# Kernel tuning notes

Measured on AMD Instinct MI355X. Metric: run time of the kernel, lower is better.

Reference implementation:

```python
import jax, jax.numpy as jnp
import numpy as np

B, N, C_IN, C_H, C_OUT, R, X_DIM = 32, 256, 64, 128, 128, 5, 1024
NEG = -9e15

def _leaky(x, s=0.2):
    return jnp.where(x >= 0, x, s * x)

def gat_layer(atoms, mask, W, b, a):
    # atoms: (B,n,c_in), mask: (B,n,n,R) bool, W: (c_in, R*c), b: (R*c,), a: (R, 2c)
    bs, n, _ = atoms.shape
    c = a.shape[1] // 2
    h = (atoms @ W + b).reshape(bs, n, R, c)            # (B,n,R,c)
    src = jnp.einsum('bnrc,rc->bnr', h, a[:, :c])       # a . h_i part
    dst = jnp.einsum('bnrc,rc->bnr', h, a[:, c:])       # a . h_j part
    logits = _leaky(src[:, :, None, :] + dst[:, None, :, :])  # (B,i,j,R)
    masked = jnp.where(mask, logits, NEG)
    probs = jax.nn.softmax(masked.reshape(bs, n, n * R), axis=2).reshape(bs, n, n, R)
    return jnp.einsum('bijr,bjrc->bic', probs, h)       # (B,n,c)

def setup_inputs() -> dict:
    key = jax.random.key(0)
    ks = jax.random.split(key, 16)
    def p(k, shape, fan):
        return jax.random.normal(k, shape, jnp.float32) * (1.414 / np.sqrt(fan))
    inp = {
        'x': jax.random.normal(ks[0], (B, X_DIM), jnp.float32),
        'y_atoms': jax.random.normal(ks[1], (B, N, C_IN), jnp.float32),
        'y_bonds': jax.random.randint(ks[2], (B, N, N, R), 0, 2, jnp.int32),
        'W1': p(ks[3], (C_IN, R * C_H), C_IN), 'b1': jnp.zeros((R * C_H,), jnp.float32),
        'a1': p(ks[4], (R, 2 * C_H), 2 * C_H),
        'W2': p(ks[5], (C_H, R * C_H), C_H), 'b2': jnp.zeros((R * C_H,), jnp.float32),
        'a2': p(ks[6], (R, 2 * C_H), 2 * C_H),
        'W3': p(ks[7], (C_H, R * C_OUT), C_H), 'b3': jnp.zeros((R * C_OUT,), jnp.float32),
        'a3': p(ks[8], (R, 2 * C_OUT), 2 * C_OUT),
        'We1': p(ks[9], (2 * C_OUT + X_DIM, 256), 2 * C_OUT + X_DIM), 'be1': jnp.zeros((256,), jnp.float32),
        'We2': p(ks[10], (256, 32), 256), 'be2': jnp.zeros((32,), jnp.float32),
        'We3': p(ks[11], (32, 1), 32), 'be3': jnp.zeros((1,), jnp.float32),
    }
    return inp

def reference(x, y_atoms, y_bonds, W1, b1, a1, W2, b2, a2, W3, b3, a3,
              We1, be1, We2, be2, We3, be3):
    mask = (y_bonds == 1)
    h = gat_layer(y_atoms, mask, W1, b1, a1)
    h = _leaky(h)                                   # dropout is identity at eval
    h = gat_layer(h, mask, W2, b2, a2)
    h = _leaky(h)
    h = gat_layer(h, mask, W3, b3, a3)
    y_feats = jnp.concatenate([jnp.mean(h, axis=1), jnp.max(h, axis=1)], axis=1)
    z = jnp.concatenate([x, y_feats], axis=1)
    z = _leaky(z @ We1 + be1)
    z = _leaky(z @ We2 + be2)
    return z @ We3 + be3
```

## Files before the change

kernel.cpp:

```cpp
#include <hip/hip_runtime.h>
#include <cstddef>

#define BB 32
#define NN 256
#define RR 5

typedef __attribute__((ext_vector_type(8))) short bf16x8;
typedef __attribute__((ext_vector_type(4))) float f32x4;

__device__ __forceinline__ float lrelu(float x) { return x >= 0.f ? x : 0.2f * x; }
__device__ __forceinline__ unsigned short f2bf(float x) {
    unsigned u = __float_as_uint(x);
    u += 0x7FFFu + ((u >> 16) & 1u);
    return (unsigned short)(u >> 16);
}

__global__ __launch_bounds__(256) void k_prep(const float* __restrict__ W1,
                                              const float* __restrict__ W2,
                                              const float* __restrict__ W3,
                                              const float* __restrict__ We1,
                                              const int* __restrict__ bonds,
                                              unsigned short* __restrict__ WT1,
                                              unsigned short* __restrict__ WT2,
                                              unsigned short* __restrict__ WT3,
                                              float* __restrict__ We1T,
                                              unsigned char* __restrict__ maskp) {
    __shared__ float Ls[40][256];
    int blk = blockIdx.x;
    int t = threadIdx.x;
    if (blk < 30) {
        int layer = blk / 10, nt = blk % 10;
        const float* W;
        unsigned short* WT;
        int K;
        if (layer == 0)      { W = W1; WT = WT1; K = 64; }
        else if (layer == 1) { W = W2; WT = WT2; K = 128; }
        else                 { W = W3; WT = WT3; K = 128; }
        int n = nt * 64 + (t & 63);
        for (int kg = (int)(t >> 6); kg < K / 8; kg += 4) {
            bf16x8 v;
#pragma unroll
            for (int e = 0; e < 8; ++e) v[e] = (short)f2bf(W[(size_t)(kg * 8 + e) * 640 + n]);
            *(bf16x8*)&WT[(size_t)n * K + kg * 8] = v;
        }
    } else if (blk < 62) {
        int bt = blk - 30;
        for (int kk = 0; kk < 40; ++kk)
            Ls[kk][t] = We1[(size_t)(bt * 40 + kk) * 256 + t];
        __syncthreads();
#pragma unroll
        for (int q = 0; q < 10; ++q) {
            float4 v;
            v.x = Ls[q * 4 + 0][t]; v.y = Ls[q * 4 + 1][t];
            v.z = Ls[q * 4 + 2][t]; v.w = Ls[q * 4 + 3][t];
            *(float4*)&We1T[(size_t)t * 1280 + bt * 40 + q * 4] = v;
        }
    } else {
        int idx = (blk - 62) * 256 + t;
        const int* p = bonds + (size_t)idx * 5;
        unsigned m = 0;
#pragma unroll
        for (int r = 0; r < 5; ++r) m |= (p[r] == 1) ? (1u << r) : 0u;
        maskp[idx] = (unsigned char)m;
    }
}

template <int K, int MODE>
__global__ __launch_bounds__(256) void k_gemm_h(const float* __restrict__ Af32,
                                                const float* __restrict__ aggP,
                                                const float* __restrict__ Zpart,
                                                const unsigned short* __restrict__ WTg,
                                                const float* __restrict__ bias,
                                                const float* __restrict__ avec,
                                                float* __restrict__ srcp,
                                                float* __restrict__ dstp,
                                                unsigned short* __restrict__ hTf) {
    const int t = threadIdx.x;
    const int n0 = blockIdx.x * 64, m0 = blockIdx.y * 64;
    const int w = t >> 6, lane = t & 63;
    const int colg = lane & 15, rquad = lane >> 4;
    const int m = m0 + w * 16 + colg;
    const int koff = rquad * 8;

    float zi = 0.f;
    if (MODE == 1) zi = 1.f / (Zpart[m] + Zpart[8192 + m]);

    f32x4 acc[4] = {};
#pragma unroll
    for (int kk = 0; kk < K; kk += 32) {
        bf16x8 af;
        size_t off = (size_t)m * K + kk + koff;
        if (MODE == 1) {
            float4 a0 = *(const float4*)&aggP[off];
            float4 a1 = *(const float4*)&aggP[off + 4];
            float4 b0 = *(const float4*)&aggP[off + 1048576];
            float4 b1 = *(const float4*)&aggP[off + 1048576 + 4];
            af[0] = (short)f2bf(lrelu((a0.x + b0.x) * zi));
            af[1] = (short)f2bf(lrelu((a0.y + b0.y) * zi));
            af[2] = (short)f2bf(lrelu((a0.z + b0.z) * zi));
            af[3] = (short)f2bf(lrelu((a0.w + b0.w) * zi));
            af[4] = (short)f2bf(lrelu((a1.x + b1.x) * zi));
            af[5] = (short)f2bf(lrelu((a1.y + b1.y) * zi));
            af[6] = (short)f2bf(lrelu((a1.z + b1.z) * zi));
            af[7] = (short)f2bf(lrelu((a1.w + b1.w) * zi));
        } else {
            float4 q0 = *(const float4*)&Af32[off];
            float4 q1 = *(const float4*)&Af32[off + 4];
            af[0] = (short)f2bf(q0.x); af[1] = (short)f2bf(q0.y);
            af[2] = (short)f2bf(q0.z); af[3] = (short)f2bf(q0.w);
            af[4] = (short)f2bf(q1.x); af[5] = (short)f2bf(q1.y);
            af[6] = (short)f2bf(q1.z); af[7] = (short)f2bf(q1.w);
        }
#pragma unroll
        for (int ct = 0; ct < 4; ++ct) {
            bf16x8 bfv = *(const bf16x8*)&WTg[(size_t)(n0 + ct * 16 + colg) * K + kk + koff];
            acc[ct] = __builtin_amdgcn_mfma_f32_16x16x32_bf16(af, bfv, acc[ct], 0, 0, 0);
        }
    }

    const int r = n0 >> 7, chalf = n0 & 127;
    const int b = m0 >> 8, jb = m0 & 255;
    float val[4][4];
    float ssum[4] = {0.f, 0.f, 0.f, 0.f}, dsum[4] = {0.f, 0.f, 0.f, 0.f};
#pragma unroll
    for (int ct = 0; ct < 4; ++ct) {
        int cg = chalf + ct * 16 + colg;
        float bv = bias[n0 + ct * 16 + colg];
        float asr = avec[r * 256 + cg];
        float ads = avec[r * 256 + 128 + cg];
#pragma unroll
        for (int reg = 0; reg < 4; ++reg) {
            float v = acc[ct][reg] + bv;
            val[ct][reg] = v;
            ssum[reg] += v * asr;
            dsum[reg] += v * ads;
        }
    }
#pragma unroll
    for (int mk = 1; mk < 16; mk <<= 1)
#pragma unroll
        for (int reg = 0; reg < 4; ++reg) {
            ssum[reg] += __shfl_xor(ssum[reg], mk);
            dsum[reg] += __shfl_xor(dsum[reg], mk);
        }
    if (colg == 0) {
        int half = (n0 >> 6) & 1;
#pragma unroll
        for (int reg = 0; reg < 4; ++reg) {
            int row = m0 + w * 16 + rquad * 4 + reg;
            srcp[half * 40960 + row * 5 + r] = ssum[reg];
            dstp[half * 40960 + row * 5 + r] = dsum[reg];
        }
    }
    {
        const int joct = (jb >> 3) + w * 2 + (rquad >> 1);
        const size_t tile = (size_t)((b * 5 + r) * 32 + joct) * 1024;
        const int sub = (rquad & 1) * 4;
#pragma unroll
        for (int ct = 0; ct < 4; ++ct) {
            int c = chalf + ct * 16 + colg;
            uint2 pk;
            pk.x = (unsigned)f2bf(val[ct][0]) | ((unsigned)f2bf(val[ct][1]) << 16);
            pk.y = (unsigned)f2bf(val[ct][2]) | ((unsigned)f2bf(val[ct][3]) << 16);
            *(uint2*)&hTf[tile + (size_t)c * 8 + sub] = pk;
        }
    }
}

__global__ __launch_bounds__(512) void k_agg(const unsigned short* __restrict__ hTf,
                                             const float* __restrict__ srcp,
                                             const float* __restrict__ dstp,
                                             const unsigned char* __restrict__ maskp,
                                             float* __restrict__ aggP,
                                             float* __restrict__ Zpart) {
    __shared__ unsigned short Ps[20480];
    __shared__ float Ss[160], Ds2l[640], Zrow[32];
    const int t = threadIdx.x;
    const int js = blockIdx.x, itile = blockIdx.y, b = blockIdx.z;
    const int ib = b * 256 + itile * 32;

    if (t < 160) Ss[t] = srcp[(size_t)ib * 5 + t] + srcp[40960 + (size_t)ib * 5 + t];
    if (t >= 160 && t < 192) Zrow[t - 160] = 0.f;
    for (int idx = t; idx < 640; idx += 512) {
        int jl = idx & 127, rr = idx >> 7;
        size_t o = (size_t)(b * 256 + js * 128 + jl) * 5 + rr;
        Ds2l[rr * 128 + jl] = dstp[o] + dstp[40960 + o];
    }
    __syncthreads();

#pragma unroll
    for (int it = 0; it < 5; ++it) {
        int p = it * 512 + t;
        int lane8 = p & 63, chunkrow = p >> 6;
        int colg8 = lane8 & 15, kq = lane8 >> 4;
        int ih = (chunkrow >= 20) ? 1 : 0;
        int s = chunkrow - ih * 20;
        int i = ih * 16 + colg8;
        int rr = s >> 2;
        int j0l = (s & 3) * 32 + kq * 8;
        uint2 mk8 = *(const uint2*)&maskp[((size_t)(ib + i) << 8) + js * 128 + j0l];
        float sv = Ss[i * 5 + rr];
        float esum = 0.f;
        bf16x8 pv;
#pragma unroll
        for (int e = 0; e < 8; ++e) {
            unsigned mb = ((e < 4 ? (mk8.x >> (8 * e)) : (mk8.y >> (8 * (e - 4)))) >> rr) & 1u;
            float v = lrelu(sv + Ds2l[rr * 128 + j0l + e]);
            float ev = mb ? __expf(v) : 0.f;
            unsigned short q = f2bf(ev);
            pv[e] = (short)q;
            esum += __uint_as_float((unsigned)q << 16);
        }
        *(bf16x8*)&Ps[p * 8] = pv;
        atomicAdd(&Zrow[i], esum);
    }
    __syncthreads();
    if (t < 32) Zpart[(size_t)js * 8192 + ib + t] = Zrow[t];

    const int w = t >> 6, lane = t & 63;
    const int ih = w & 1, ch = w >> 1;
    const int colg = lane & 15, rquad = lane >> 4;
    f32x4 acc[2] = {};
    const size_t bbase = (size_t)(b * 5) * 32 * 1024;
#pragma unroll
    for (int s = 0; s < 20; ++s) {
        bf16x8 af = *(const bf16x8*)&Ps[((ih * 20 + s) * 64 + lane) * 8];
        const int rr = s >> 2;
        const int joct = js * 16 + (s & 3) * 4 + rquad;
        const size_t tbase = bbase + (size_t)(rr * 32 + joct) * 1024;
#pragma unroll
        for (int ct = 0; ct < 2; ++ct) {
            int c = ch * 32 + ct * 16 + colg;
            bf16x8 bfv = *(const bf16x8*)&hTf[tbase + (size_t)c * 8];
            acc[ct] = __builtin_amdgcn_mfma_f32_16x16x32_bf16(af, bfv, acc[ct], 0, 0, 0);
        }
    }
    float* op = aggP + (size_t)js * 1048576;
    const int irow = ib + ih * 16 + rquad * 4;
#pragma unroll
    for (int ct = 0; ct < 2; ++ct) {
        int c = ch * 32 + ct * 16 + colg;
#pragma unroll
        for (int reg = 0; reg < 4; ++reg)
            op[(size_t)(irow + reg) * 128 + c] = acc[ct][reg];
    }
}

__global__ __launch_bounds__(256) void k_pool(const float* __restrict__ aggP,
                                              const float* __restrict__ Zpart,
                                              float* __restrict__ poolS,
                                              float* __restrict__ poolM) {
    int nc = blockIdx.x, b = blockIdx.y;
    int t = threadIdx.x;
    int c = t & 127, sub = t >> 7;
    __shared__ float Zl[32];
    __shared__ float Sh[2][128], Mh[2][128];
    if (t < 32) {
        int rowg = b * 256 + nc * 32 + t;
        Zl[t] = 1.f / (Zpart[rowg] + Zpart[8192 + rowg]);
    }
    __syncthreads();
    float sm = 0.f, mx = -3.4e38f;
#pragma unroll
    for (int nn = 0; nn < 16; ++nn) {
        int nl = sub * 16 + nn;
        size_t o = (size_t)(b * 256 + nc * 32 + nl) * 128 + c;
        float v = (aggP[o] + aggP[o + 1048576]) * Zl[nl];
        sm += v; mx = fmaxf(mx, v);
    }
    Sh[sub][c] = sm; Mh[sub][c] = mx;
    __syncthreads();
    if (t < 128) {
        poolS[(b * 8 + nc) * 128 + t] = Sh[0][t] + Sh[1][t];
        poolM[(b * 8 + nc) * 128 + t] = fmaxf(Mh[0][t], Mh[1][t]);
    }
}

__global__ __launch_bounds__(256) void k_mlp1(const float* __restrict__ x,
                                              const float* __restrict__ poolS,
                                              const float* __restrict__ poolM,
                                              const float* __restrict__ We1T,
                                              const float* __restrict__ be1,
                                              float* __restrict__ z1g) {
    int og = blockIdx.x, b = blockIdx.y;
    int t = threadIdx.x;
    __shared__ float zs[1280];
    for (int i = t; i < 1024; i += 256) zs[i] = x[b * 1024 + i];
    if (t < 128) {
        float s = 0.f;
#pragma unroll
        for (int nc = 0; nc < 8; ++nc) s += poolS[(b * 8 + nc) * 128 + t];
        zs[1024 + t] = s * (1.f / 256.f);
    } else {
        int f = t - 128;
        float mx = -3.4e38f;
#pragma unroll
        for (int nc = 0; nc < 8; ++nc) mx = fmaxf(mx, poolM[(b * 8 + nc) * 128 + f]);
        zs[1152 + f] = mx;
    }
    __syncthreads();
    int w = t >> 6, lane = t & 63;
#pragma unroll
    for (int oo = 0; oo < 4; ++oo) {
        int o = og * 16 + w * 4 + oo;
        float s = 0.f;
#pragma unroll
        for (int i = 0; i < 20; ++i) {
            int k = i * 64 + lane;
            s += zs[k] * We1T[(size_t)o * 1280 + k];
        }
#pragma unroll
        for (int off = 32; off > 0; off >>= 1) s += __shfl_down(s, off);
        if (lane == 0) z1g[b * 256 + o] = lrelu(s + be1[o]);
    }
}

__global__ __launch_bounds__(256) void k_mlp23(const float* __restrict__ z1g,
                                               const float* __restrict__ We2,
                                               const float* __restrict__ be2,
                                               const float* __restrict__ We3,
                                               const float* __restrict__ be3,
                                               float* __restrict__ out) {
    int b = blockIdx.x, t = threadIdx.x;
    __shared__ float zs[256], z2s[32];
    zs[t] = z1g[b * 256 + t];
    __syncthreads();
    if (t < 32) {
        float s2 = be2[t];
        for (int k = 0; k < 256; ++k) s2 += zs[k] * We2[k * 32 + t];
        z2s[t] = lrelu(s2);
    }
    __syncthreads();
    if (t == 0) {
        float s3 = be3[0];
#pragma unroll
        for (int k = 0; k < 32; ++k) s3 += z2s[k] * We3[k];
        out[b] = s3;
    }
}

constexpr size_t O_MASK  = 0;
constexpr size_t O_SRCP  = 2097152;
constexpr size_t O_DSTP  = O_SRCP + 2ull * 40960 * 4;
constexpr size_t O_AGG   = O_DSTP + 2ull * 40960 * 4;
constexpr size_t O_ZP    = O_AGG + 2ull * 1048576 * 4;
constexpr size_t O_HT    = O_ZP + 2ull * 8192 * 4;
constexpr size_t O_WT1   = O_HT + 5242880ull * 2;
constexpr size_t O_WT2   = O_WT1 + 640ull * 64 * 2;
constexpr size_t O_WT3   = O_WT2 + 640ull * 128 * 2;
constexpr size_t O_WE1T  = O_WT3 + 640ull * 128 * 2;
constexpr size_t O_POOLS = O_WE1T + 256ull * 1280 * 4;
constexpr size_t O_POOLM = O_POOLS + 32ull * 8 * 128 * 4;
constexpr size_t O_Z1    = O_POOLM + 32ull * 8 * 128 * 4;

extern "C" void kernel_launch(void* const* d_in, const int* in_sizes, int n_in,
                              void* d_out, int out_size, void* d_ws, size_t ws_size,
                              hipStream_t stream) {
    const float* x       = (const float*)d_in[0];
    const float* y_atoms = (const float*)d_in[1];
    const int*   y_bonds = (const int*)d_in[2];
    const float* W1 = (const float*)d_in[3];
    const float* b1 = (const float*)d_in[4];
    const float* a1 = (const float*)d_in[5];
    const float* W2 = (const float*)d_in[6];
    const float* b2 = (const float*)d_in[7];
    const float* a2 = (const float*)d_in[8];
    const float* W3 = (const float*)d_in[9];
    const float* b3 = (const float*)d_in[10];
    const float* a3 = (const float*)d_in[11];
    const float* We1 = (const float*)d_in[12];
    const float* be1 = (const float*)d_in[13];
    const float* We2 = (const float*)d_in[14];
    const float* be2 = (const float*)d_in[15];
    const float* We3 = (const float*)d_in[16];
    const float* be3 = (const float*)d_in[17];
    float* out = (float*)d_out;

    char* ws = (char*)d_ws;
    unsigned char* maskp = (unsigned char*)(ws + O_MASK);
    float* srcp = (float*)(ws + O_SRCP);
    float* dstp = (float*)(ws + O_DSTP);
    float* aggP = (float*)(ws + O_AGG);
    float* Zpart = (float*)(ws + O_ZP);
    unsigned short* hTf = (unsigned short*)(ws + O_HT);
    unsigned short* WT1 = (unsigned short*)(ws + O_WT1);
    unsigned short* WT2 = (unsigned short*)(ws + O_WT2);
    unsigned short* WT3 = (unsigned short*)(ws + O_WT3);
    float* We1T  = (float*)(ws + O_WE1T);
    float* poolS = (float*)(ws + O_POOLS);
    float* poolM = (float*)(ws + O_POOLM);
    float* z1g   = (float*)(ws + O_Z1);

    dim3 blk(256);

    k_prep<<<8254, blk, 0, stream>>>(W1, W2, W3, We1, y_bonds, WT1, WT2, WT3, We1T, maskp);

    k_gemm_h<64, 0><<<dim3(10, 128), blk, 0, stream>>>(
        y_atoms, nullptr, nullptr, WT1, b1, a1, srcp, dstp, hTf);
    k_agg<<<dim3(2, 8, 32), dim3(512), 0, stream>>>(hTf, srcp, dstp, maskp, aggP, Zpart);

    k_gemm_h<128, 1><<<dim3(10, 128), blk, 0, stream>>>(
        nullptr, aggP, Zpart, WT2, b2, a2, srcp, dstp, hTf);
    k_agg<<<dim3(2, 8, 32), dim3(512), 0, stream>>>(hTf, srcp, dstp, maskp, aggP, Zpart);

    k_gemm_h<128, 1><<<dim3(10, 128), blk, 0, stream>>>(
        nullptr, aggP, Zpart, WT3, b3, a3, srcp, dstp, hTf);
    k_agg<<<dim3(2, 8, 32), dim3(512), 0, stream>>>(hTf, srcp, dstp, maskp, aggP, Zpart);

    k_pool<<<dim3(8, 32), blk, 0, stream>>>(aggP, Zpart, poolS, poolM);
    k_mlp1<<<dim3(16, 32), blk, 0, stream>>>(x, poolS, poolM, We1T, be1, z1g);
    k_mlp23<<<32, blk, 0, stream>>>(z1g, We2, be2, We3, be3, out);
}
```

Baseline: 233.5 us.

## Fuse all GAT stages into one cooperative persistent kernel with grid syncs

Replaces the chain of eleven separate kernel launches (prep, three gemm/agg pairs, pool, two MLP kernels) with a single cooperative persistent kernel. Stages are separated by grid.sync() and work is distributed over virtual blocks in grid-stride loops. The mask packing is also vectorized to write 8 bytes per thread. This removes per-launch overhead and inter-kernel gaps. In exchange it adds grid-wide barrier cost and caps the grid at occupancy-limited size, which can cut parallelism in the gemm and agg phases.

```diff
diff --git a/kernel.cpp b/kernel.cpp
--- a/kernel.cpp
+++ b/kernel.cpp
@@ -1,9 +1,8 @@
 #include <hip/hip_runtime.h>
+#include <hip/hip_cooperative_groups.h>
 #include <cstddef>
 
-#define BB 32
-#define NN 256
-#define RR 5
+namespace cg = cooperative_groups;
 
 typedef __attribute__((ext_vector_type(8))) short bf16x8;
 typedef __attribute__((ext_vector_type(4))) float f32x4;
@@ -15,327 +14,370 @@
     return (unsigned short)(u >> 16);
 }
 
-__global__ __launch_bounds__(256) void k_prep(const float* __restrict__ W1,
-                                              const float* __restrict__ W2,
-                                              const float* __restrict__ W3,
-                                              const float* __restrict__ We1,
-                                              const int* __restrict__ bonds,
-                                              unsigned short* __restrict__ WT1,
-                                              unsigned short* __restrict__ WT2,
-                                              unsigned short* __restrict__ WT3,
-                                              float* __restrict__ We1T,
-                                              unsigned char* __restrict__ maskp) {
-    __shared__ float Ls[40][256];
-    int blk = blockIdx.x;
-    int t = threadIdx.x;
-    if (blk < 30) {
-        int layer = blk / 10, nt = blk % 10;
-        const float* W;
-        unsigned short* WT;
-        int K;
-        if (layer == 0)      { W = W1; WT = WT1; K = 64; }
-        else if (layer == 1) { W = W2; WT = WT2; K = 128; }
-        else                 { W = W3; WT = WT3; K = 128; }
-        int n = nt * 64 + (t & 63);
-        for (int kg = (int)(t >> 6); kg < K / 8; kg += 4) {
-            bf16x8 v;
-#pragma unroll
-            for (int e = 0; e < 8; ++e) v[e] = (short)f2bf(W[(size_t)(kg * 8 + e) * 640 + n]);
-            *(bf16x8*)&WT[(size_t)n * K + kg * 8] = v;
-        }
-    } else if (blk < 62) {
-        int bt = blk - 30;
-        for (int kk = 0; kk < 40; ++kk)
-            Ls[kk][t] = We1[(size_t)(bt * 40 + kk) * 256 + t];
-        __syncthreads();
-#pragma unroll
-        for (int q = 0; q < 10; ++q) {
-            float4 v;
-            v.x = Ls[q * 4 + 0][t]; v.y = Ls[q * 4 + 1][t];
-            v.z = Ls[q * 4 + 2][t]; v.w = Ls[q * 4 + 3][t];
-            *(float4*)&We1T[(size_t)t * 1280 + bt * 40 + q * 4] = v;
-        }
-    } else {
-        int idx = (blk - 62) * 256 + t;
-        const int* p = bonds + (size_t)idx * 5;
-        unsigned m = 0;
-#pragma unroll
-        for (int r = 0; r < 5; ++r) m |= (p[r] == 1) ? (1u << r) : 0u;
-        maskp[idx] = (unsigned char)m;
+template <int K, int MODE>
+__device__ __forceinline__ void gemm_phase(
+    int blk, int nvb, int t,
+    const float* __restrict__ Af32, const float* __restrict__ aggP,
+    const float* __restrict__ Zpart, const unsigned short* __restrict__ WTg,
+    const float* __restrict__ bias, const float* __restrict__ avec,
+    float* __restrict__ srcp, float* __restrict__ dstp,
+    unsigned short* __restrict__ hTf)
+{
+    const int su = t >> 8, tl = t & 255;
+    const int w = tl >> 6, lane = tl & 63;
+    const int colg = lane & 15, rquad = lane >> 4;
+    const int koff = rquad * 8;
+    for (int U = blk * 2 + su; U < 1280; U += nvb * 2) {
+        const int n0 = (U >> 7) * 64, m0 = (U & 127) * 64;
+        const int m = m0 + w * 16 + colg;
+        float zi = 0.f;
+        if (MODE == 1) zi = 1.f / (Zpart[m] + Zpart[8192 + m]);
+        f32x4 acc[4] = {};
+#pragma unroll
+        for (int kk = 0; kk < K; kk += 32) {
+            bf16x8 af;
+            size_t off = (size_t)m * K + kk + koff;
+            if (MODE == 1) {
+                float4 a0 = *(const float4*)&aggP[off];
+                float4 a1 = *(const float4*)&aggP[off + 4];
+                float4 b0 = *(const float4*)&aggP[off + 1048576];
+                float4 b1 = *(const float4*)&aggP[off + 1048576 + 4];
+                af[0] = (short)f2bf(lrelu((a0.x + b0.x) * zi));
+                af[1] = (short)f2bf(lrelu((a0.y + b0.y) * zi));
+                af[2] = (short)f2bf(lrelu((a0.z + b0.z) * zi));
+                af[3] = (short)f2bf(lrelu((a0.w + b0.w) * zi));
+                af[4] = (short)f2bf(lrelu((a1.x + b1.x) * zi));
+                af[5] = (short)f2bf(lrelu((a1.y + b1.y) * zi));
+                af[6] = (short)f2bf(lrelu((a1.z + b1.z) * zi));
+                af[7] = (short)f2bf(lrelu((a1.w + b1.w) * zi));
+            } else {
+                float4 q0 = *(const float4*)&Af32[off];
+                float4 q1 = *(const float4*)&Af32[off + 4];
+                af[0] = (short)f2bf(q0.x); af[1] = (short)f2bf(q0.y);
+                af[2] = (short)f2bf(q0.z); af[3] = (short)f2bf(q0.w);
+                af[4] = (short)f2bf(q1.x); af[5] = (short)f2bf(q1.y);
+                af[6] = (short)f2bf(q1.z); af[7] = (short)f2bf(q1.w);
+            }
+#pragma unroll
+            for (int ct = 0; ct < 4; ++ct) {
+                bf16x8 bfv = *(const bf16x8*)&WTg[(size_t)(n0 + ct * 16 + colg) * K + kk + koff];
+                acc[ct] = __builtin_amdgcn_mfma_f32_16x16x32_bf16(af, bfv, acc[ct], 0, 0, 0);
+            }
+        }
+        const int r = n0 >> 7, chalf = n0 & 127;
+        const int b = m0 >> 8, jb = m0 & 255;
+        float val[4][4];
+        float ssum[4] = {0.f, 0.f, 0.f, 0.f}, dsum[4] = {0.f, 0.f, 0.f, 0.f};
+#pragma unroll
+        for (int ct = 0; ct < 4; ++ct) {
+            int cg2 = chalf + ct * 16 + colg;
+            float bv = bias[n0 + ct * 16 + colg];
+            float asr = avec[r * 256 + cg2];
+            float ads = avec[r * 256 + 128 + cg2];
+#pragma unroll
+            for (int reg = 0; reg < 4; ++reg) {
+                float v = acc[ct][reg] + bv;
+                val[ct][reg] = v;
+                ssum[reg] += v * asr;
+                dsum[reg] += v * ads;
+            }
+        }
+#pragma unroll
+        for (int mk = 1; mk < 16; mk <<= 1)
+#pragma unroll
+            for (int reg = 0; reg < 4; ++reg) {
+                ssum[reg] += __shfl_xor(ssum[reg], mk);
+                dsum[reg] += __shfl_xor(dsum[reg], mk);
+            }
+        if (colg == 0) {
+            int half = (n0 >> 6) & 1;
+#pragma unroll
+            for (int reg = 0; reg < 4; ++reg) {
+                int row = m0 + w * 16 + rquad * 4 + reg;
+                srcp[half * 40960 + row * 5 + r] = ssum[reg];
+                dstp[half * 40960 + row * 5 + r] = dsum[reg];
+            }
+        }
+        {
+            const int joct = (jb >> 3) + w * 2 + (rquad >> 1);
+            const size_t tile = (size_t)((b * 5 + r) * 32 + joct) * 1024;
+            const int sub = (rquad & 1) * 4;
+#pragma unroll
+            for (int ct = 0; ct < 4; ++ct) {
+                int c = chalf + ct * 16 + colg;
+                uint2 pk;
+                pk.x = (unsigned)f2bf(val[ct][0]) | ((unsigned)f2bf(val[ct][1]) << 16);
+                pk.y = (unsigned)f2bf(val[ct][2]) | ((unsigned)f2bf(val[ct][3]) << 16);
+                *(uint2*)&hTf[tile + (size_t)c * 8 + sub] = pk;
+            }
+        }
     }
 }
 
-template <int K, int MODE>
-__global__ __launch_bounds__(256) void k_gemm_h(const float* __restrict__ Af32,
-                                                const float* __restrict__ aggP,
-                                                const float* __restrict__ Zpart,
-                                                const unsigned short* __restrict__ WTg,
-                                                const float* __restrict__ bias,
-                                                const float* __restrict__ avec,
-                                                float* __restrict__ srcp,
-                                                float* __restrict__ dstp,
-                                                unsigned short* __restrict__ hTf) {
-    const int t = threadIdx.x;
-    const int n0 = blockIdx.x * 64, m0 = blockIdx.y * 64;
-    const int w = t >> 6, lane = t & 63;
-    const int colg = lane & 15, rquad = lane >> 4;
-    const int m = m0 + w * 16 + colg;
-    const int koff = rquad * 8;
-
-    float zi = 0.f;
-    if (MODE == 1) zi = 1.f / (Zpart[m] + Zpart[8192 + m]);
-
-    f32x4 acc[4] = {};
-#pragma unroll
-    for (int kk = 0; kk < K; kk += 32) {
-        bf16x8 af;
-        size_t off = (size_t)m * K + kk + koff;
-        if (MODE == 1) {
-            float4 a0 = *(const float4*)&aggP[off];
-            float4 a1 = *(const float4*)&aggP[off + 4];
-            float4 b0 = *(const float4*)&aggP[off + 1048576];
-            float4 b1 = *(const float4*)&aggP[off + 1048576 + 4];
-            af[0] = (short)f2bf(lrelu((a0.x + b0.x) * zi));
-            af[1] = (short)f2bf(lrelu((a0.y + b0.y) * zi));
-            af[2] = (short)f2bf(lrelu((a0.z + b0.z) * zi));
-            af[3] = (short)f2bf(lrelu((a0.w + b0.w) * zi));
-            af[4] = (short)f2bf(lrelu((a1.x + b1.x) * zi));
-            af[5] = (short)f2bf(lrelu((a1.y + b1.y) * zi));
-            af[6] = (short)f2bf(lrelu((a1.z + b1.z) * zi));
-            af[7] = (short)f2bf(lrelu((a1.w + b1.w) * zi));
-        } else {
-            float4 q0 = *(const float4*)&Af32[off];
-            float4 q1 = *(const float4*)&Af32[off + 4];
-            af[0] = (short)f2bf(q0.x); af[1] = (short)f2bf(q0.y);
-            af[2] = (short)f2bf(q0.z); af[3] = (short)f2bf(q0.w);
-            af[4] = (short)f2bf(q1.x); af[5] = (short)f2bf(q1.y);
-            af[6] = (short)f2bf(q1.z); af[7] = (short)f2bf(q1.w);
-        }
-#pragma unroll
-        for (int ct = 0; ct < 4; ++ct) {
-            bf16x8 bfv = *(const bf16x8*)&WTg[(size_t)(n0 + ct * 16 + colg) * K + kk + koff];
-            acc[ct] = __builtin_amdgcn_mfma_f32_16x16x32_bf16(af, bfv, acc[ct], 0, 0, 0);
-        }
-    }
-
-    const int r = n0 >> 7, chalf = n0 & 127;
-    const int b = m0 >> 8, jb = m0 & 255;
-    float val[4][4];
-    float ssum[4] = {0.f, 0.f, 0.f, 0.f}, dsum[4] = {0.f, 0.f, 0.f, 0.f};
-#pragma unroll
-    for (int ct = 0; ct < 4; ++ct) {
-        int cg = chalf + ct * 16 + colg;
-        float bv = bias[n0 + ct * 16 + colg];
-        float asr = avec[r * 256 + cg];
-        float ads = avec[r * 256 + 128 + cg];
-#pragma unroll
-        for (int reg = 0; reg < 4; ++reg) {
-            float v = acc[ct][reg] + bv;
-            val[ct][reg] = v;
-            ssum[reg] += v * asr;
-            dsum[reg] += v * ads;
-        }
-    }
-#pragma unroll
-    for (int mk = 1; mk < 16; mk <<= 1)
-#pragma unroll
-        for (int reg = 0; reg < 4; ++reg) {
-            ssum[reg] += __shfl_xor(ssum[reg], mk);
-            dsum[reg] += __shfl_xor(dsum[reg], mk);
-        }
-    if (colg == 0) {
-        int half = (n0 >> 6) & 1;
-#pragma unroll
-        for (int reg = 0; reg < 4; ++reg) {
-            int row = m0 + w * 16 + rquad * 4 + reg;
-            srcp[half * 40960 + row * 5 + r] = ssum[reg];
-            dstp[half * 40960 + row * 5 + r] = dsum[reg];
-        }
-    }
-    {
-        const int joct = (jb >> 3) + w * 2 + (rquad >> 1);
-        const size_t tile = (size_t)((b * 5 + r) * 32 + joct) * 1024;
-        const int sub = (rquad & 1) * 4;
-#pragma unroll
-        for (int ct = 0; ct < 4; ++ct) {
-            int c = chalf + ct * 16 + colg;
-            uint2 pk;
-            pk.x = (unsigned)f2bf(val[ct][0]) | ((unsigned)f2bf(val[ct][1]) << 16);
-            pk.y = (unsigned)f2bf(val[ct][2]) | ((unsigned)f2bf(val[ct][3]) << 16);
-            *(uint2*)&hTf[tile + (size_t)c * 8 + sub] = pk;
-        }
-    }
-}
-
-__global__ __launch_bounds__(512) void k_agg(const unsigned short* __restrict__ hTf,
-                                             const float* __restrict__ srcp,
-                                             const float* __restrict__ dstp,
-                                             const unsigned char* __restrict__ maskp,
-                                             float* __restrict__ aggP,
-                                             float* __restrict__ Zpart) {
-    __shared__ unsigned short Ps[20480];
-    __shared__ float Ss[160], Ds2l[640], Zrow[32];
-    const int t = threadIdx.x;
-    const int js = blockIdx.x, itile = blockIdx.y, b = blockIdx.z;
-    const int ib = b * 256 + itile * 32;
-
-    if (t < 160) Ss[t] = srcp[(size_t)ib * 5 + t] + srcp[40960 + (size_t)ib * 5 + t];
-    if (t >= 160 && t < 192) Zrow[t - 160] = 0.f;
-    for (int idx = t; idx < 640; idx += 512) {
-        int jl = idx & 127, rr = idx >> 7;
-        size_t o = (size_t)(b * 256 + js * 128 + jl) * 5 + rr;
-        Ds2l[rr * 128 + jl] = dstp[o] + dstp[40960 + o];
-    }
-    __syncthreads();
-
-#pragma unroll
-    for (int it = 0; it < 5; ++it) {
-        int p = it * 512 + t;
-        int lane8 = p & 63, chunkrow = p >> 6;
-        int colg8 = lane8 & 15, kq = lane8 >> 4;
-        int ih = (chunkrow >= 20) ? 1 : 0;
-        int s = chunkrow - ih * 20;
-        int i = ih * 16 + colg8;
-        int rr = s >> 2;
-        int j0l = (s & 3) * 32 + kq * 8;
-        uint2 mk8 = *(const uint2*)&maskp[((size_t)(ib + i) << 8) + js * 128 + j0l];
-        float sv = Ss[i * 5 + rr];
-        float esum = 0.f;
-        bf16x8 pv;
-#pragma unroll
-        for (int e = 0; e < 8; ++e) {
-            unsigned mb = ((e < 4 ? (mk8.x >> (8 * e)) : (mk8.y >> (8 * (e - 4)))) >> rr) & 1u;
-            float v = lrelu(sv + Ds2l[rr * 128 + j0l + e]);
-            float ev = mb ? __expf(v) : 0.f;
-            unsigned short q = f2bf(ev);
-            pv[e] = (short)q;
-            esum += __uint_as_float((unsigned)q << 16);
-        }
-        *(bf16x8*)&Ps[p * 8] = pv;
-        atomicAdd(&Zrow[i], esum);
-    }
-    __syncthreads();
-    if (t < 32) Zpart[(size_t)js * 8192 + ib + t] = Zrow[t];
-
-    const int w = t >> 6, lane = t & 63;
-    const int ih = w & 1, ch = w >> 1;
-    const int colg = lane & 15, rquad = lane >> 4;
-    f32x4 acc[2] = {};
-    const size_t bbase = (size_t)(b * 5) * 32 * 1024;
-#pragma unroll
-    for (int s = 0; s < 20; ++s) {
-        bf16x8 af = *(const bf16x8*)&Ps[((ih * 20 + s) * 64 + lane) * 8];
-        const int rr = s >> 2;
-        const int joct = js * 16 + (s & 3) * 4 + rquad;
-        const size_t tbase = bbase + (size_t)(rr * 32 + joct) * 1024;
+__device__ __forceinline__ void agg_phase(
+    int blk, int nvb, int t, char* smem,
+    const unsigned short* __restrict__ hTf,
+    const float* __restrict__ srcp, const float* __restrict__ dstp,
+    const unsigned char* __restrict__ maskp,
+    float* __restrict__ aggP, float* __restrict__ Zpart)
+{
+    unsigned short* Ps = (unsigned short*)smem;
+    float* Ss = (float*)(smem + 40960);
+    float* Ds2l = (float*)(smem + 41600);
+    float* Zrow = (float*)(smem + 44160);
+    for (int vb = blk; vb < 512; vb += nvb) {
+        const int js = vb & 1, itile = (vb >> 1) & 7, b = vb >> 4;
+        const int ib = b * 256 + itile * 32;
+        __syncthreads();
+        if (t < 160) Ss[t] = srcp[(size_t)ib * 5 + t] + srcp[40960 + (size_t)ib * 5 + t];
+        if (t >= 160 && t < 192) Zrow[t - 160] = 0.f;
+        for (int idx = t; idx < 640; idx += 512) {
+            int jl = idx & 127, rr = idx >> 7;
+            size_t o = (size_t)(b * 256 + js * 128 + jl) * 5 + rr;
+            Ds2l[rr * 128 + jl] = dstp[o] + dstp[40960 + o];
+        }
+        __syncthreads();
+#pragma unroll
+        for (int it = 0; it < 5; ++it) {
+            int p = it * 512 + t;
+            int lane8 = p & 63, chunkrow = p >> 6;
+            int colg8 = lane8 & 15, kq = lane8 >> 4;
+            int ih = (chunkrow >= 20) ? 1 : 0;
+            int s = chunkrow - ih * 20;
+            int i = ih * 16 + colg8;
+            int rr = s >> 2;
+            int j0l = (s & 3) * 32 + kq * 8;
+            uint2 mk8 = *(const uint2*)&maskp[((size_t)(ib + i) << 8) + js * 128 + j0l];
+            float sv = Ss[i * 5 + rr];
+            float esum = 0.f;
+            bf16x8 pv;
+#pragma unroll
+            for (int e = 0; e < 8; ++e) {
+                unsigned mb = ((e < 4 ? (mk8.x >> (8 * e)) : (mk8.y >> (8 * (e - 4)))) >> rr) & 1u;
+                float v = lrelu(sv + Ds2l[rr * 128 + j0l + e]);
+                float ev = mb ? __expf(v) : 0.f;
+                unsigned short q = f2bf(ev);
+                pv[e] = (short)q;
+                esum += __uint_as_float((unsigned)q << 16);
+            }
+            *(bf16x8*)&Ps[p * 8] = pv;
+            atomicAdd(&Zrow[i], esum);
+        }
+        __syncthreads();
+        if (t < 32) Zpart[(size_t)js * 8192 + ib + t] = Zrow[t];
+
+        const int w = t >> 6, lane = t & 63;
+        const int ih = w & 1, ch = w >> 1;
+        const int colg = lane & 15, rquad = lane >> 4;
+        f32x4 acc[2] = {};
+        const size_t bbase = (size_t)(b * 5) * 32 * 1024;
+#pragma unroll
+        for (int s = 0; s < 20; ++s) {
+            bf16x8 af = *(const bf16x8*)&Ps[((ih * 20 + s) * 64 + lane) * 8];
+            const int rr = s >> 2;
+            const int joct = js * 16 + (s & 3) * 4 + rquad;
+            const size_t tbase = bbase + (size_t)(rr * 32 + joct) * 1024;
+#pragma unroll
+            for (int ct = 0; ct < 2; ++ct) {
+                int c = ch * 32 + ct * 16 + colg;
+                bf16x8 bfv = *(const bf16x8*)&hTf[tbase + (size_t)c * 8];
+                acc[ct] = __builtin_amdgcn_mfma_f32_16x16x32_bf16(af, bfv, acc[ct], 0, 0, 0);
+            }
+        }
+        float* op = aggP + (size_t)js * 1048576;
+        const int irow = ib + ih * 16 + rquad * 4;
 #pragma unroll
         for (int ct = 0; ct < 2; ++ct) {
             int c = ch * 32 + ct * 16 + colg;
-            bf16x8 bfv = *(const bf16x8*)&hTf[tbase + (size_t)c * 8];
-            acc[ct] = __builtin_amdgcn_mfma_f32_16x16x32_bf16(af, bfv, acc[ct], 0, 0, 0);
-        }
-    }
-    float* op = aggP + (size_t)js * 1048576;
-    const int irow = ib + ih * 16 + rquad * 4;
-#pragma unroll
-    for (int ct = 0; ct < 2; ++ct) {
-        int c = ch * 32 + ct * 16 + colg;
-#pragma unroll
-        for (int reg = 0; reg < 4; ++reg)
-            op[(size_t)(irow + reg) * 128 + c] = acc[ct][reg];
+#pragma unroll
+            for (int reg = 0; reg < 4; ++reg)
+                op[(size_t)(irow + reg) * 128 + c] = acc[ct][reg];
+        }
     }
 }
 
-__global__ __launch_bounds__(256) void k_pool(const float* __restrict__ aggP,
-                                              const float* __restrict__ Zpart,
-                                              float* __restrict__ poolS,
-                                              float* __restrict__ poolM) {
-    int nc = blockIdx.x, b = blockIdx.y;
-    int t = threadIdx.x;
-    int c = t & 127, sub = t >> 7;
-    __shared__ float Zl[32];
-    __shared__ float Sh[2][128], Mh[2][128];
-    if (t < 32) {
-        int rowg = b * 256 + nc * 32 + t;
-        Zl[t] = 1.f / (Zpart[rowg] + Zpart[8192 + rowg]);
-    }
-    __syncthreads();
-    float sm = 0.f, mx = -3.4e38f;
-#pragma unroll
-    for (int nn = 0; nn < 16; ++nn) {
-        int nl = sub * 16 + nn;
-        size_t o = (size_t)(b * 256 + nc * 32 + nl) * 128 + c;
-        float v = (aggP[o] + aggP[o + 1048576]) * Zl[nl];
-        sm += v; mx = fmaxf(mx, v);
-    }
-    Sh[sub][c] = sm; Mh[sub][c] = mx;
-    __syncthreads();
-    if (t < 128) {
-        poolS[(b * 8 + nc) * 128 + t] = Sh[0][t] + Sh[1][t];
-        poolM[(b * 8 + nc) * 128 + t] = fmaxf(Mh[0][t], Mh[1][t]);
-    }
-}
-
-__global__ __launch_bounds__(256) void k_mlp1(const float* __restrict__ x,
-                                              const float* __restrict__ poolS,
-                                              const float* __restrict__ poolM,
-                                              const float* __restrict__ We1T,
-                                              const float* __restrict__ be1,
-                                              float* __restrict__ z1g) {
-    int og = blockIdx.x, b = blockIdx.y;
-    int t = threadIdx.x;
-    __shared__ float zs[1280];
-    for (int i = t; i < 1024; i += 256) zs[i] = x[b * 1024 + i];
-    if (t < 128) {
-        float s = 0.f;
-#pragma unroll
-        for (int nc = 0; nc < 8; ++nc) s += poolS[(b * 8 + nc) * 128 + t];
-        zs[1024 + t] = s * (1.f / 256.f);
-    } else {
-        int f = t - 128;
-        float mx = -3.4e38f;
-#pragma unroll
-        for (int nc = 0; nc < 8; ++nc) mx = fmaxf(mx, poolM[(b * 8 + nc) * 128 + f]);
-        zs[1152 + f] = mx;
-    }
-    __syncthreads();
-    int w = t >> 6, lane = t & 63;
-#pragma unroll
-    for (int oo = 0; oo < 4; ++oo) {
-        int o = og * 16 + w * 4 + oo;
-        float s = 0.f;
-#pragma unroll
-        for (int i = 0; i < 20; ++i) {
-            int k = i * 64 + lane;
-            s += zs[k] * We1T[(size_t)o * 1280 + k];
-        }
-#pragma unroll
-        for (int off = 32; off > 0; off >>= 1) s += __shfl_down(s, off);
-        if (lane == 0) z1g[b * 256 + o] = lrelu(s + be1[o]);
-    }
-}
-
-__global__ __launch_bounds__(256) void k_mlp23(const float* __restrict__ z1g,
-                                               const float* __restrict__ We2,
-                                               const float* __restrict__ be2,
-                                               const float* __restrict__ We3,
-                                               const float* __restrict__ be3,
-                                               float* __restrict__ out) {
-    int b = blockIdx.x, t = threadIdx.x;
-    __shared__ float zs[256], z2s[32];
-    zs[t] = z1g[b * 256 + t];
-    __syncthreads();
-    if (t < 32) {
-        float s2 = be2[t];
-        for (int k = 0; k < 256; ++k) s2 += zs[k] * We2[k * 32 + t];
-        z2s[t] = lrelu(s2);
-    }
-    __syncthreads();
-    if (t == 0) {
-        float s3 = be3[0];
-#pragma unroll
-        for (int k = 0; k < 32; ++k) s3 += z2s[k] * We3[k];
-        out[b] = s3;
+__global__ __launch_bounds__(512, 4) void k_mega(
+    const float* __restrict__ x, const float* __restrict__ y_atoms,
+    const int* __restrict__ bonds,
+    const float* __restrict__ W1, const float* __restrict__ b1, const float* __restrict__ a1,
+    const float* __restrict__ W2, const float* __restrict__ b2, const float* __restrict__ a2,
+    const float* __restrict__ W3, const float* __restrict__ b3, const float* __restrict__ a3,
+    const float* __restrict__ We1, const float* __restrict__ be1,
+    const float* __restrict__ We2, const float* __restrict__ be2,
+    const float* __restrict__ We3, const float* __restrict__ be3,
+    unsigned short* __restrict__ WT1, unsigned short* __restrict__ WT2,
+    unsigned short* __restrict__ WT3, float* __restrict__ We1T,
+    unsigned char* __restrict__ maskp,
+    float* __restrict__ srcp, float* __restrict__ dstp,
+    float* __restrict__ aggP, float* __restrict__ Zpart,
+    unsigned short* __restrict__ hTf,
+    float* __restrict__ poolS, float* __restrict__ poolM,
+    float* __restrict__ z1g, float* __restrict__ out)
+{
+    __shared__ __align__(16) char smem[44288];
+    cg::grid_group grid = cg::this_grid();
+    const int blk = blockIdx.x;
+    const int nvb = gridDim.x;
+    const int t = threadIdx.x;
+
+    for (int vb = blk; vb < 62; vb += nvb) {
+        if (vb < 30) {
+            if (t < 256) {
+                int layer = vb / 10, nt = vb % 10;
+                const float* W; unsigned short* WT; int K;
+                if (layer == 0)      { W = W1; WT = WT1; K = 64; }
+                else if (layer == 1) { W = W2; WT = WT2; K = 128; }
+                else                 { W = W3; WT = WT3; K = 128; }
+                int n = nt * 64 + (t & 63);
+                for (int kg = (t >> 6); kg < K / 8; kg += 4) {
+                    bf16x8 v;
+#pragma unroll
+                    for (int e = 0; e < 8; ++e) v[e] = (short)f2bf(W[(size_t)(kg * 8 + e) * 640 + n]);
+                    *(bf16x8*)&WT[(size_t)n * K + kg * 8] = v;
+                }
+            }
+        } else {
+            int bt = vb - 30;
+            float* Ls = (float*)smem;
+            __syncthreads();
+            if (t < 256) {
+                for (int kk = 0; kk < 40; ++kk)
+                    Ls[kk * 256 + t] = We1[(size_t)(bt * 40 + kk) * 256 + t];
+            }
+            __syncthreads();
+            if (t < 256) {
+#pragma unroll
+                for (int q = 0; q < 10; ++q) {
+                    float4 v;
+                    v.x = Ls[(q * 4 + 0) * 256 + t]; v.y = Ls[(q * 4 + 1) * 256 + t];
+                    v.z = Ls[(q * 4 + 2) * 256 + t]; v.w = Ls[(q * 4 + 3) * 256 + t];
+                    *(float4*)&We1T[(size_t)t * 1280 + bt * 40 + q * 4] = v;
+                }
+            }
+        }
+    }
+    {
+        const size_t step = (size_t)nvb * 512 * 8;
+        for (size_t base = ((size_t)blk * 512 + t) * 8; base < 2097152ull; base += step) {
+            unsigned mb[8];
+#pragma unroll
+            for (int e = 0; e < 8; ++e) {
+                const int* p = bonds + (base + e) * 5;
+                unsigned m = 0;
+#pragma unroll
+                for (int r = 0; r < 5; ++r) m |= (p[r] == 1) ? (1u << r) : 0u;
+                mb[e] = m;
+            }
+            uint2 pk;
+            pk.x = mb[0] | (mb[1] << 8) | (mb[2] << 16) | (mb[3] << 24);
+            pk.y = mb[4] | (mb[5] << 8) | (mb[6] << 16) | (mb[7] << 24);
+            *(uint2*)&maskp[base] = pk;
+        }
+    }
+    grid.sync();
+
+    gemm_phase<64, 0>(blk, nvb, t, y_atoms, nullptr, nullptr, WT1, b1, a1, srcp, dstp, hTf);
+    grid.sync();
+    agg_phase(blk, nvb, t, smem, hTf, srcp, dstp, maskp, aggP, Zpart);
+    grid.sync();
+    gemm_phase<128, 1>(blk, nvb, t, nullptr, aggP, Zpart, WT2, b2, a2, srcp, dstp, hTf);
+    grid.sync();
+    agg_phase(blk, nvb, t, smem, hTf, srcp, dstp, maskp, aggP, Zpart);
+    grid.sync();
+    gemm_phase<128, 1>(blk, nvb, t, nullptr, aggP, Zpart, WT3, b3, a3, srcp, dstp, hTf);
+    grid.sync();
+    agg_phase(blk, nvb, t, smem, hTf, srcp, dstp, maskp, aggP, Zpart);
+    grid.sync();
+
+    {
+        const int su = t >> 8, tl = t & 255;
+        for (int U = blk * 2 + su; U < 256; U += nvb * 2) {
+            const int nc = U & 7, b = U >> 3;
+            float* Zl = (float*)smem + su * 32;
+            float* Sh = (float*)smem + 64 + su * 256;
+            float* Mh = (float*)smem + 64 + 512 + su * 256;
+            const int c = tl & 127, sub = tl >> 7;
+            __syncthreads();
+            if (tl < 32) {
+                int rowg = b * 256 + nc * 32 + tl;
+                Zl[tl] = 1.f / (Zpart[rowg] + Zpart[8192 + rowg]);
+            }
+            __syncthreads();
+            float sm = 0.f, mx = -3.4e38f;
+#pragma unroll
+            for (int nn = 0; nn < 16; ++nn) {
+                int nl = sub * 16 + nn;
+                size_t o = (size_t)(b * 256 + nc * 32 + nl) * 128 + c;
+                float v = (aggP[o] + aggP[o + 1048576]) * Zl[nl];
+                sm += v; mx = fmaxf(mx, v);
+            }
+            Sh[sub * 128 + c] = sm; Mh[sub * 128 + c] = mx;
+            __syncthreads();
+            if (tl < 128) {
+                poolS[(b * 8 + nc) * 128 + tl] = Sh[tl] + Sh[128 + tl];
+                poolM[(b * 8 + nc) * 128 + tl] = fmaxf(Mh[tl], Mh[128 + tl]);
+            }
+        }
+    }
+    grid.sync();
+
+    for (int vb = blk; vb < 512; vb += nvb) {
+        const int og = vb & 15, b = vb >> 4;
+        float* zs = (float*)smem;
+        __syncthreads();
+        if (t < 256) {
+            for (int i = t; i < 1024; i += 256) zs[i] = x[b * 1024 + i];
+            if (t < 128) {
+                float s = 0.f;
+#pragma unroll
+                for (int nc2 = 0; nc2 < 8; ++nc2) s += poolS[(b * 8 + nc2) * 128 + t];
+                zs[1024 + t] = s * (1.f / 256.f);
+            } else {
+                int f = t - 128;
+                float mx = -3.4e38f;
+#pragma unroll
+                for (int nc2 = 0; nc2 < 8; ++nc2) mx = fmaxf(mx, poolM[(b * 8 + nc2) * 128 + f]);
+                zs[1152 + f] = mx;
+            }
+        }
+        __syncthreads();
+        if (t < 256) {
+            int w2 = t >> 6, lane2 = t & 63;
+#pragma unroll
+            for (int oo = 0; oo < 4; ++oo) {
+                int o = og * 16 + w2 * 4 + oo;
+                float s = 0.f;
+#pragma unroll
+                for (int i = 0; i < 20; ++i) {
+                    int k = i * 64 + lane2;
+                    s += zs[k] * We1T[(size_t)o * 1280 + k];
+                }
+#pragma unroll
+                for (int off = 32; off > 0; off >>= 1) s += __shfl_down(s, off);
+                if (lane2 == 0) z1g[b * 256 + o] = lrelu(s + be1[o]);
+            }
+        }
+    }
+    grid.sync();
+
+    for (int vb = blk; vb < 32; vb += nvb) {
+        float* zs = (float*)smem;
+        float* z2s = (float*)smem + 256;
+        __syncthreads();
+        if (t < 256) zs[t] = z1g[vb * 256 + t];
+        __syncthreads();
+        if (t < 32) {
+            float s2 = be2[t];
+            for (int k = 0; k < 256; ++k) s2 += zs[k] * We2[k * 32 + t];
+            z2s[t] = lrelu(s2);
+        }
+        __syncthreads();
+        if (t == 0) {
+            float s3 = be3[0];
+#pragma unroll
+            for (int k = 0; k < 32; ++k) s3 += z2s[k] * We3[k];
+            out[vb] = s3;
+        }
     }
 }
 
@@ -391,23 +433,24 @@
     float* poolM = (float*)(ws + O_POOLM);
     float* z1g   = (float*)(ws + O_Z1);
 
-    dim3 blk(256);
-
-    k_prep<<<8254, blk, 0, stream>>>(W1, W2, W3, We1, y_bonds, WT1, WT2, WT3, We1T, maskp);
-
-    k_gemm_h<64, 0><<<dim3(10, 128), blk, 0, stream>>>(
-        y_atoms, nullptr, nullptr, WT1, b1, a1, srcp, dstp, hTf);
-    k_agg<<<dim3(2, 8, 32), dim3(512), 0, stream>>>(hTf, srcp, dstp, maskp, aggP, Zpart);
-
-    k_gemm_h<128, 1><<<dim3(10, 128), blk, 0, stream>>>(
-        nullptr, aggP, Zpart, WT2, b2, a2, srcp, dstp, hTf);
-    k_agg<<<dim3(2, 8, 32), dim3(512), 0, stream>>>(hTf, srcp, dstp, maskp, aggP, Zpart);
-
-    k_gemm_h<128, 1><<<dim3(10, 128), blk, 0, stream>>>(
-        nullptr, aggP, Zpart, WT3, b3, a3, srcp, dstp, hTf);
-    k_agg<<<dim3(2, 8, 32), dim3(512), 0, stream>>>(hTf, srcp, dstp, maskp, aggP, Zpart);
-
-    k_pool<<<dim3(8, 32), blk, 0, stream>>>(aggP, Zpart, poolS, poolM);
-    k_mlp1<<<dim3(16, 32), blk, 0, stream>>>(x, poolS, poolM, We1T, be1, z1g);
-    k_mlp23<<<32, blk, 0, stream>>>(z1g, We2, be2, We3, be3, out);
+    int maxPerCU = 0;
+    hipOccupancyMaxActiveBlocksPerMultiprocessor(&maxPerCU, (const void*)k_mega, 512, 0);
+    int nblocks = maxPerCU * 256;
+    if (nblocks > 512) nblocks = 512;
+    if (nblocks < 1) nblocks = 256;
+
+    void* args[] = {
+        (void*)&x, (void*)&y_atoms, (void*)&y_bonds,
+        (void*)&W1, (void*)&b1, (void*)&a1,
+        (void*)&W2, (void*)&b2, (void*)&a2,
+        (void*)&W3, (void*)&b3, (void*)&a3,
+        (void*)&We1, (void*)&be1, (void*)&We2, (void*)&be2,
+        (void*)&We3, (void*)&be3,
+        (void*)&WT1, (void*)&WT2, (void*)&WT3, (void*)&We1T,
+        (void*)&maskp,
+        (void*)&srcp, (void*)&dstp, (void*)&aggP, (void*)&Zpart,
+        (void*)&hTf,
+        (void*)&poolS, (void*)&poolM, (void*)&z1g, (void*)&out
+    };
+    hipLaunchCooperativeKernel((const void*)k_mega, dim3(nblocks), dim3(512), args, 0, stream);
 }
```

After: 578.5 us. 2.48x slower.

## Halve k_agg row tile to 16 rows and fuse MLP head kernels

Applied to the files above, without the earlier changes.

The aggregation kernel now processes 16 rows per block with 256 threads instead of 32 rows with 512. That doubles the grid and halves LDS use per block, with each thread computing probabilities for one row across five iterations. The two MLP kernels are merged into a single per-batch head kernel, which removes one launch and the z1 round trip through global memory. In exchange, the first MLP layer now runs on only 32 blocks, each looping over 256 outputs, which serialises that work. The smaller agg tiles also reload the hTf B-operand twice as often.

```diff
diff --git a/kernel.cpp b/kernel.cpp
--- a/kernel.cpp
+++ b/kernel.cpp
@@ -167,79 +167,78 @@
     }
 }
 
-__global__ __launch_bounds__(512) void k_agg(const unsigned short* __restrict__ hTf,
+__global__ __launch_bounds__(256) void k_agg(const unsigned short* __restrict__ hTf,
                                              const float* __restrict__ srcp,
                                              const float* __restrict__ dstp,
                                              const unsigned char* __restrict__ maskp,
                                              float* __restrict__ aggP,
                                              float* __restrict__ Zpart) {
-    __shared__ unsigned short Ps[20480];
-    __shared__ float Ss[160], Ds2l[640], Zrow[32];
+    __shared__ unsigned short Ps[10240];
+    __shared__ float Ss[80], Ds2l[640], Zrow[16];
     const int t = threadIdx.x;
     const int js = blockIdx.x, itile = blockIdx.y, b = blockIdx.z;
-    const int ib = b * 256 + itile * 32;
-
-    if (t < 160) Ss[t] = srcp[(size_t)ib * 5 + t] + srcp[40960 + (size_t)ib * 5 + t];
-    if (t >= 160 && t < 192) Zrow[t - 160] = 0.f;
-    for (int idx = t; idx < 640; idx += 512) {
+    const int ib = b * 256 + itile * 16;
+
+    if (t < 80) Ss[t] = srcp[(size_t)ib * 5 + t] + srcp[40960 + (size_t)ib * 5 + t];
+    if (t >= 80 && t < 96) Zrow[t - 80] = 0.f;
+    for (int idx = t; idx < 640; idx += 256) {
         int jl = idx & 127, rr = idx >> 7;
         size_t o = (size_t)(b * 256 + js * 128 + jl) * 5 + rr;
         Ds2l[rr * 128 + jl] = dstp[o] + dstp[40960 + o];
     }
     __syncthreads();
 
-#pragma unroll
-    for (int it = 0; it < 5; ++it) {
-        int p = it * 512 + t;
-        int lane8 = p & 63, chunkrow = p >> 6;
-        int colg8 = lane8 & 15, kq = lane8 >> 4;
-        int ih = (chunkrow >= 20) ? 1 : 0;
-        int s = chunkrow - ih * 20;
-        int i = ih * 16 + colg8;
-        int rr = s >> 2;
-        int j0l = (s & 3) * 32 + kq * 8;
-        uint2 mk8 = *(const uint2*)&maskp[((size_t)(ib + i) << 8) + js * 128 + j0l];
-        float sv = Ss[i * 5 + rr];
+    {
+        const int i = t & 15;
         float esum = 0.f;
-        bf16x8 pv;
-#pragma unroll
-        for (int e = 0; e < 8; ++e) {
-            unsigned mb = ((e < 4 ? (mk8.x >> (8 * e)) : (mk8.y >> (8 * (e - 4)))) >> rr) & 1u;
-            float v = lrelu(sv + Ds2l[rr * 128 + j0l + e]);
-            float ev = mb ? __expf(v) : 0.f;
-            unsigned short q = f2bf(ev);
-            pv[e] = (short)q;
-            esum += __uint_as_float((unsigned)q << 16);
-        }
-        *(bf16x8*)&Ps[p * 8] = pv;
+#pragma unroll
+        for (int it = 0; it < 5; ++it) {
+            int p = it * 256 + t;
+            int lane8 = p & 63, s = p >> 6;
+            int kq = lane8 >> 4;
+            int k0 = s * 32 + kq * 8;
+            int rr = k0 >> 7, j0l = k0 & 127;
+            uint2 mk8 = *(const uint2*)&maskp[((size_t)(ib + i) << 8) + js * 128 + j0l];
+            float sv = Ss[i * 5 + rr];
+            bf16x8 pv;
+#pragma unroll
+            for (int e = 0; e < 8; ++e) {
+                unsigned mb = ((e < 4 ? (mk8.x >> (8 * e)) : (mk8.y >> (8 * (e - 4)))) >> rr) & 1u;
+                float v = lrelu(sv + Ds2l[rr * 128 + j0l + e]);
+                float ev = mb ? __expf(v) : 0.f;
+                unsigned short q = f2bf(ev);
+                pv[e] = (short)q;
+                esum += __uint_as_float((unsigned)q << 16);
+            }
+            *(bf16x8*)&Ps[p * 8] = pv;
+        }
         atomicAdd(&Zrow[i], esum);
     }
     __syncthreads();
-    if (t < 32) Zpart[(size_t)js * 8192 + ib + t] = Zrow[t];
+    if (t < 16) Zpart[(size_t)js * 8192 + ib + t] = Zrow[t];
 
     const int w = t >> 6, lane = t & 63;
-    const int ih = w & 1, ch = w >> 1;
     const int colg = lane & 15, rquad = lane >> 4;
     f32x4 acc[2] = {};
     const size_t bbase = (size_t)(b * 5) * 32 * 1024;
 #pragma unroll
     for (int s = 0; s < 20; ++s) {
-        bf16x8 af = *(const bf16x8*)&Ps[((ih * 20 + s) * 64 + lane) * 8];
+        bf16x8 af = *(const bf16x8*)&Ps[(s * 64 + lane) * 8];
         const int rr = s >> 2;
         const int joct = js * 16 + (s & 3) * 4 + rquad;
         const size_t tbase = bbase + (size_t)(rr * 32 + joct) * 1024;
 #pragma unroll
         for (int ct = 0; ct < 2; ++ct) {
-            int c = ch * 32 + ct * 16 + colg;
+            int c = w * 32 + ct * 16 + colg;
             bf16x8 bfv = *(const bf16x8*)&hTf[tbase + (size_t)c * 8];
             acc[ct] = __builtin_amdgcn_mfma_f32_16x16x32_bf16(af, bfv, acc[ct], 0, 0, 0);
         }
     }
     float* op = aggP + (size_t)js * 1048576;
-    const int irow = ib + ih * 16 + rquad * 4;
+    const int irow = ib + rquad * 4;
 #pragma unroll
     for (int ct = 0; ct < 2; ++ct) {
-        int c = ch * 32 + ct * 16 + colg;
+        int c = w * 32 + ct * 16 + colg;
 #pragma unroll
         for (int reg = 0; reg < 4; ++reg)
             op[(size_t)(irow + reg) * 128 + c] = acc[ct][reg];
@@ -276,15 +275,18 @@
     }
 }
 
-__global__ __launch_bounds__(256) void k_mlp1(const float* __restrict__ x,
+__global__ __launch_bounds__(256) void k_head(const float* __restrict__ x,
                                               const float* __restrict__ poolS,
                                               const float* __restrict__ poolM,
                                               const float* __restrict__ We1T,
                                               const float* __restrict__ be1,
-                                              float* __restrict__ z1g) {
-    int og = blockIdx.x, b = blockIdx.y;
-    int t = threadIdx.x;
-    __shared__ float zs[1280];
+                                              const float* __restrict__ We2,
+                                              const float* __restrict__ be2,
+                                              const float* __restrict__ We3,
+                                              const float* __restrict__ be3,
+                                              float* __restrict__ out) {
+    int b = blockIdx.x, t = threadIdx.x;
+    __shared__ float zs[1280], z1s[256], z2s[32];
     for (int i = t; i < 1024; i += 256) zs[i] = x[b * 1024 + i];
     if (t < 128) {
         float s = 0.f;
@@ -301,33 +303,25 @@
     __syncthreads();
     int w = t >> 6, lane = t & 63;
 #pragma unroll
-    for (int oo = 0; oo < 4; ++oo) {
-        int o = og * 16 + w * 4 + oo;
-        float s = 0.f;
-#pragma unroll
-        for (int i = 0; i < 20; ++i) {
-            int k = i * 64 + lane;
-            s += zs[k] * We1T[(size_t)o * 1280 + k];
-        }
-#pragma unroll
-        for (int off = 32; off > 0; off >>= 1) s += __shfl_down(s, off);
-        if (lane == 0) z1g[b * 256 + o] = lrelu(s + be1[o]);
-    }
-}
-
-__global__ __launch_bounds__(256) void k_mlp23(const float* __restrict__ z1g,
-                                               const float* __restrict__ We2,
-                                               const float* __restrict__ be2,
-                                               const float* __restrict__ We3,
-                                               const float* __restrict__ be3,
-                                               float* __restrict__ out) {
-    int b = blockIdx.x, t = threadIdx.x;
-    __shared__ float zs[256], z2s[32];
-    zs[t] = z1g[b * 256 + t];
+    for (int pass = 0; pass < 16; ++pass) {
+#pragma unroll
+        for (int oo = 0; oo < 4; ++oo) {
+            int o = pass * 16 + w * 4 + oo;
+            float s = 0.f;
+#pragma unroll
+            for (int i = 0; i < 20; ++i) {
+                int k = i * 64 + lane;
+                s += zs[k] * We1T[(size_t)o * 1280 + k];
+            }
+#pragma unroll
+            for (int off = 32; off > 0; off >>= 1) s += __shfl_down(s, off);
+            if (lane == 0) z1s[o] = lrelu(s + be1[o]);
+        }
+    }
     __syncthreads();
     if (t < 32) {
         float s2 = be2[t];
-        for (int k = 0; k < 256; ++k) s2 += zs[k] * We2[k * 32 + t];
+        for (int k = 0; k < 256; ++k) s2 += z1s[k] * We2[k * 32 + t];
         z2s[t] = lrelu(s2);
     }
     __syncthreads();
@@ -351,7 +345,6 @@
 constexpr size_t O_WE1T  = O_WT3 + 640ull * 128 * 2;
 constexpr size_t O_POOLS = O_WE1T + 256ull * 1280 * 4;
 constexpr size_t O_POOLM = O_POOLS + 32ull * 8 * 128 * 4;
-constexpr size_t O_Z1    = O_POOLM + 32ull * 8 * 128 * 4;
 
 extern "C" void kernel_launch(void* const* d_in, const int* in_sizes, int n_in,
                               void* d_out, int out_size, void* d_ws, size_t ws_size,
@@ -389,7 +382,6 @@
     float* We1T  = (float*)(ws + O_WE1T);
     float* poolS = (float*)(ws + O_POOLS);
     float* poolM = (float*)(ws + O_POOLM);
-    float* z1g   = (float*)(ws + O_Z1);
 
     dim3 blk(256);
 
@@ -397,17 +389,16 @@
 
     k_gemm_h<64, 0><<<dim3(10, 128), blk, 0, stream>>>(
         y_atoms, nullptr, nullptr, WT1, b1, a1, srcp, dstp, hTf);
-    k_agg<<<dim3(2, 8, 32), dim3(512), 0, stream>>>(hTf, srcp, dstp, maskp, aggP, Zpart);
+    k_agg<<<dim3(2, 16, 32), blk, 0, stream>>>(hTf, srcp, dstp, maskp, aggP, Zpart);
 
     k_gemm_h<128, 1><<<dim3(10, 128), blk, 0, stream>>>(
         nullptr, aggP, Zpart, WT2, b2, a2, srcp, dstp, hTf);
-    k_agg<<<dim3(2, 8, 32), dim3(512), 0, stream>>>(hTf, srcp, dstp, maskp, aggP, Zpart);
+    k_agg<<<dim3(2, 16, 32), blk, 0, stream>>>(hTf, srcp, dstp, maskp, aggP, Zpart);
 
     k_gemm_h<128, 1><<<dim3(10, 128), blk, 0, stream>>>(
         nullptr, aggP, Zpart, WT3, b3, a3, srcp, dstp, hTf);
-    k_agg<<<dim3(2, 8, 32), dim3(512), 0, stream>>>(hTf, srcp, dstp, maskp, aggP, Zpart);
+    k_agg<<<dim3(2, 16, 32), blk, 0, stream>>>(hTf, srcp, dstp, maskp, aggP, Zpart);
 
     k_pool<<<dim3(8, 32), blk, 0, stream>>>(aggP, Zpart, poolS, poolM);
-    k_mlp1<<<dim3(16, 32), blk, 0, stream>>>(x, poolS, poolM, We1T, be1, z1g);
-    k_mlp23<<<32, blk, 0, stream>>>(z1g, We2, be2, We3, be3, out);
-}
+    k_head<<<32, blk, 0, stream>>>(x, poolS, poolM, We1T, be1, We2, be2, We3, be3, out);
+}
```

Measured after the change: 264.7 us. 13.3% more time.
